# Kernel tuning notes

Measured on AMD Instinct MI355X. Metric: run time of the kernel, lower is better.

## Reference

```python
import jax, jax.numpy as jnp
import numpy as np

STATE_DIM = 16
MEAS_DIM = 8
T = 500_000


def setup_inputs() -> dict:
    key = jax.random.key(0)
    k1, k2 = jax.random.split(key)
    measurements = jax.random.normal(k1, (T, MEAS_DIM, 1), dtype=jnp.float32)
    # F contracted slightly below identity so the 500k-step recursion stays stable
    F = 0.95 * jnp.eye(STATE_DIM, dtype=jnp.float32) \
        + 0.01 * jax.random.normal(k2, (STATE_DIM, STATE_DIM), dtype=jnp.float32)
    H = jnp.eye(MEAS_DIM, STATE_DIM, dtype=jnp.float32)  # matches nn.Parameter(torch.eye(m, n))
    Q = jnp.eye(STATE_DIM, dtype=jnp.float32)
    R = jnp.eye(MEAS_DIM, dtype=jnp.float32)
    return {"measurements": measurements, "F": F, "H": H, "Q": Q, "R": R}


def reference(measurements, F, H, Q, R):
    n = F.shape[0]
    I = jnp.eye(n, dtype=F.dtype)
    x0 = jnp.zeros((n, 1), dtype=F.dtype)   # self.x init
    P0 = jnp.eye(n, dtype=F.dtype)          # self.P init

    def step(carry, z):
        x, P = carry
        # predict
        x = F @ x
        P = F @ P @ F.T + Q
        # update
        y = z - H @ x                         # (m,1) innovation
        S = H @ P @ H.T + R                   # (m,m) innovation covariance
        K = P @ H.T @ jnp.linalg.inv(S)       # (n,m) Kalman gain (faithful to torch.linalg.inv)
        x = x + K @ y
        P = (I - K @ H) @ P
        return (x, P), x

    _, states = jax.lax.scan(step, (x0, P0), measurements)
    return states  # (T, n, 1)
```

## Files before the change

### kernel.cpp

```cpp
#include <hip/hip_runtime.h>


#define TT 500000
#define T0 40
#define L1 32
#define NCHUNK 15624
#define GH 16
#define OWN 32
#define NBLK2 489

#define OFF_A    0
#define OFF_KR   256
#define OFF_AL   512
#define OFF_KH   784

#define FENCE_LDS() do { \
  asm volatile("s_waitcnt lgkmcnt(0)" ::: "memory"); \
  __builtin_amdgcn_sched_barrier(0); \
} while (0)

#define FMACDPP(d, x, a, S) \
  asm("v_fmac_f32_dpp %0, %1, %2 row_ror:" #S " row_mask:0xf bank_mask:0xf" \
      : "+v"(d) : "v"(x), "v"(a))
#define MULDPPD(d, x, a, dep, S) \
  asm("v_mul_f32_dpp %0, %1, %2 row_ror:" #S " row_mask:0xf bank_mask:0xf" \
      : "=v"(d) : "v"(x), "v"(a), "v"(dep))

__device__ __forceinline__ float rlf(float v, int lane) {
  return __int_as_float(__builtin_amdgcn_readlane(__float_as_int(v), lane));
}
__device__ __forceinline__ float bpermf(int byteaddr, float v) {
  return __int_as_float(__builtin_amdgcn_ds_bpermute(byteaddr, __float_as_int(v)));
}
template<int CTL> __device__ __forceinline__ float dppf(float x) {
  return __int_as_float(__builtin_amdgcn_update_dpp(
      0, __float_as_int(x), CTL, 0xF, 0xF, false));
}
#define QP1 0x39
#define QP2 0x4E
#define QP3 0x93

__device__ __forceinline__ int rot_dir() {
  int r = threadIdx.x & 15;
  int m = __builtin_amdgcn_update_dpp(0, r, 0x121, 0xF, 0xF, false);
  return (m - r) & 15;
}
__device__ __forceinline__ float mv16(const float a[16], float x) {
  float s0 = a[0] * x;
  float s1, s2, s3;
  MULDPPD(s1, x, a[1], s0, 1);
  MULDPPD(s2, x, a[2], s0, 2);
  MULDPPD(s3, x, a[3], s0, 3);
  FMACDPP(s0, x, a[4], 4);   FMACDPP(s1, x, a[5], 5);
  FMACDPP(s2, x, a[6], 6);   FMACDPP(s3, x, a[7], 7);
  FMACDPP(s0, x, a[8], 8);   FMACDPP(s1, x, a[9], 9);
  FMACDPP(s2, x, a[10], 10); FMACDPP(s3, x, a[11], 11);
  FMACDPP(s0, x, a[12], 12); FMACDPP(s1, x, a[13], 13);
  FMACDPP(s2, x, a[14], 14); FMACDPP(s3, x, a[15], 15);
  return (s0 + s1) + (s2 + s3);
}
__device__ __forceinline__ float stepAK(const float a[16], const float k8[8],
                                        float u, float zv) {
  float s0 = __builtin_fmaf(k8[0], zv, a[0] * u);
  float s1, s2, s3;
  MULDPPD(s1, u, a[1], s0, 1);
  MULDPPD(s2, u, a[2], s0, 2);
  MULDPPD(s3, u, a[3], s0, 3);
  FMACDPP(s0, u, a[4], 4);   FMACDPP(s1, u, a[5], 5);
  FMACDPP(s2, u, a[6], 6);   FMACDPP(s3, u, a[7], 7);
  FMACDPP(s0, u, a[8], 8);   FMACDPP(s1, u, a[9], 9);
  FMACDPP(s2, u, a[10], 10); FMACDPP(s3, u, a[11], 11);
  FMACDPP(s0, u, a[12], 12); FMACDPP(s1, u, a[13], 13);
  FMACDPP(s2, u, a[14], 14); FMACDPP(s3, u, a[15], 15);
  FMACDPP(s1, zv, k8[1], 1); FMACDPP(s2, zv, k8[2], 2);
  FMACDPP(s3, zv, k8[3], 3); FMACDPP(s0, zv, k8[4], 4);
  FMACDPP(s1, zv, k8[5], 5); FMACDPP(s2, zv, k8[6], 6);
  FMACDPP(s3, zv, k8[7], 7);
  return (s0 + s1) + (s2 + s3);
}
__device__ __forceinline__ void load16(const float* p, int r, float d[16]) {
  #pragma unroll
  for (int j = 0; j < 4; ++j) {
    float4 t = ((const float4*)p)[r*4 + j];
    d[4*j] = t.x; d[4*j+1] = t.y; d[4*j+2] = t.z; d[4*j+3] = t.w;
  }
}
__device__ __forceinline__ void loadkrf(const float* p, int r, float k8[8]) {
  float kr[16];
  load16(p, r, kr);
  #pragma unroll
  for (int i = 0; i < 8; ++i) k8[i] = kr[i] + kr[i + 8];
}
__device__ __forceinline__ void loadz(const float* __restrict__ z, int s0_,
                                      int rr, float zr[L1]) {
  const float* zp = z + (size_t)s0_ * 8 + (rr & 7);
  if (s0_ + L1 <= TT) {
    #pragma unroll
    for (int t = 0; t < L1; ++t) zr[t] = zp[t * 8];
  } else {
    #pragma unroll
    for (int t = 0; t < L1; ++t) {
      const float* q = (s0_ + t < TT) ? (zp + t * 8) : z;
      zr[t] = *q;
    }
  }
}

__global__ __launch_bounds__(64) void kf_ricc(
    const float* __restrict__ Fg, const float* __restrict__ Qg,
    const float* __restrict__ Rg, float* __restrict__ ws)
{
  const int l  = threadIdx.x;
  const int r4 = l >> 2;
  const int q  = l & 3;
  const int c4 = q * 4;
  const int dir = rot_dir();

  __shared__ float Ps[16][20], Pbs[16][20], Ms[16][20];
  __shared__ float KsL[16][8];

  float frow[16];
  #pragma unroll
  for (int k = 0; k < 16; ++k) frow[k] = Fg[r4*16 + k];
  float4 ftr[16];
  #pragma unroll
  for (int d = 0; d < 4; ++d) {
    #pragma unroll
    for (int jp = 0; jp < 4; ++jp) {
      int col = 4*((q + d) & 3) + jp;
      ftr[d*4+jp] = make_float4(Fg[(c4+0)*16 + col], Fg[(c4+1)*16 + col],
                                Fg[(c4+2)*16 + col], Fg[(c4+3)*16 + col]);
    }
  }
  float4 qreg = *(const float4*)&Qg[r4*16 + c4];
  float rcol[8];
  {
    int cc = l & 7;
    #pragma unroll
    for (int i = 0; i < 8; ++i) rcol[i] = Rg[i*8 + cc];
  }
  *(float4*)&Ps[r4][c4] = make_float4(r4==c4 ?1.f:0.f, r4==c4+1?1.f:0.f,
                                      r4==c4+2?1.f:0.f, r4==c4+3?1.f:0.f);
  const int  cidx = (l < 8) ? l : ((l < 24) ? (l - 8) : (l & 7));
  const bool isS  = (l < 8);
  const bool isB  = (l >= 8 && l < 24);
  const int  bj   = l - 8;
  const int  ba   = (8 + r4) << 2;
  float v[8];
  FENCE_LDS();

  for (int t = 0; t < T0; ++t) {
    float m0=0.f,m1=0.f,m2=0.f,m3=0.f;
    #pragma unroll
    for (int k = 0; k < 16; ++k) {
      float4 pk = *(const float4*)&Ps[k][c4];
      float f = frow[k];
      m0 += f*pk.x; m1 += f*pk.y; m2 += f*pk.z; m3 += f*pk.w;
    }
    float g1x=dppf<QP1>(m0), g1y=dppf<QP1>(m1), g1z=dppf<QP1>(m2), g1w=dppf<QP1>(m3);
    float g2x=dppf<QP2>(m0), g2y=dppf<QP2>(m1), g2z=dppf<QP2>(m2), g2w=dppf<QP2>(m3);
    float g3x=dppf<QP3>(m0), g3y=dppf<QP3>(m1), g3z=dppf<QP3>(m2), g3w=dppf<QP3>(m3);
    const float mq[4][4] = {{m0,m1,m2,m3},{g1x,g1y,g1z,g1w},
                            {g2x,g2y,g2z,g2w},{g3x,g3y,g3z,g3w}};
    float b0=qreg.x, b1=qreg.y, b2=qreg.z, b3=qreg.w;
    #pragma unroll
    for (int d = 0; d < 4; ++d) {
      #pragma unroll
      for (int jp = 0; jp < 4; ++jp) {
        float mm = mq[d][jp];
        float4 ft = ftr[d*4+jp];
        b0 += mm*ft.x; b1 += mm*ft.y; b2 += mm*ft.z; b3 += mm*ft.w;
      }
    }
    float4 pb = make_float4(b0,b1,b2,b3);
    *(float4*)&Pbs[r4][c4] = pb;
    FENCE_LDS();
    #pragma unroll
    for (int i = 0; i < 8; ++i)
      v[i] = Pbs[i][cidx] + (isS ? rcol[i] : 0.f);
    #pragma unroll
    for (int p = 0; p < 8; ++p) {
      float piv = rlf(v[p], p);
      float rc  = __builtin_amdgcn_rcpf(piv);
      float fi[8];
      #pragma unroll
      for (int i = 0; i < 8; ++i) fi[i] = rlf(v[i], p) * rc;
      #pragma unroll
      for (int i = 0; i < 8; ++i) if (i != p) v[i] -= fi[i] * v[p];
    }
    {
      float dv[8];
      #pragma unroll
      for (int i = 0; i < 8; ++i) dv[i] = __builtin_amdgcn_rcpf(rlf(v[i], i));
      #pragma unroll
      for (int i = 0; i < 8; ++i) v[i] *= dv[i];
    }
    if (isB) {
      #pragma unroll
      for (int i = 0; i < 8; ++i) ws[OFF_KH + t*128 + bj*8 + i] = v[i];
    }
    float kk[8];
    #pragma unroll
    for (int i = 0; i < 8; ++i) kk[i] = bpermf(ba, v[i]);
    float4 pn = pb;
    #pragma unroll
    for (int k = 0; k < 8; ++k) {
      float4 pr = *(const float4*)&Pbs[k][c4];
      float kv = kk[k];
      pn.x -= kv*pr.x; pn.y -= kv*pr.y; pn.z -= kv*pr.z; pn.w -= kv*pr.w;
    }
    *(float4*)&Ps[r4][c4] = pn;
    FENCE_LDS();
  }

  if (isB) {
    #pragma unroll
    for (int i = 0; i < 8; ++i) KsL[bj][i] = v[i];
  }
  float kk[8];
  #pragma unroll
  for (int i = 0; i < 8; ++i) kk[i] = bpermf(ba, v[i]);
  float a[4];
  #pragma unroll
  for (int j = 0; j < 4; ++j) {
    float s = Fg[r4*16 + c4 + j];
    #pragma unroll
    for (int k = 0; k < 8; ++k) s -= kk[k] * Fg[k*16 + c4 + j];
    a[j] = s;
  }
  *(float4*)&Ms[r4][c4] = make_float4(a[0],a[1],a[2],a[3]);
  #pragma unroll
  for (int j = 0; j < 4; ++j) {
    int c = c4 + j;
    int s = ((c - r4) * dir) & 15;
    ws[OFF_A + r4*16 + s] = a[j];
  }
  FENCE_LDS();
  if (l < 16) {
    #pragma unroll
    for (int s = 0; s < 16; ++s) {
      int c = (l + s*dir) & 15;
      ws[OFF_KR + l*16 + s] = (c < 8) ? KsL[l][c] : 0.f;
    }
  }
  FENCE_LDS();
  for (int n = 0; n < 5; ++n) {
    float (*src)[20] = (n & 1) ? Pbs : Ms;
    float (*dst)[20] = (n & 1) ? Ms : Pbs;
    float b[4] = {0.f, 0.f, 0.f, 0.f};
    #pragma unroll
    for (int k = 0; k < 16; ++k) {
      float m = src[r4][k];
      const float* p = &src[k][c4];
      b[0] += m*p[0]; b[1] += m*p[1]; b[2] += m*p[2]; b[3] += m*p[3];
    }
    FENCE_LDS();
    dst[r4][c4]=b[0]; dst[r4][c4+1]=b[1]; dst[r4][c4+2]=b[2]; dst[r4][c4+3]=b[3];
    FENCE_LDS();
    if (n == 4) {
      #pragma unroll
      for (int j = 0; j < 4; ++j) {
        int c = c4 + j;
        int s = ((c - r4) * dir) & 15;
        ws[OFF_AL + r4*16 + s] = b[j];
      }
    }
  }
}

__global__ __launch_bounds__(768) void kf_scan(
    const float* __restrict__ z, const float* __restrict__ Fg,
    float* __restrict__ ws, float* __restrict__ out)
{
  const int tid = threadIdx.x;
  const int bid = blockIdx.x;
  const int r = tid & 15;
  const int g = tid >> 4;

  __shared__ float ueL[48 * 16];
  __shared__ float X0s[16];

  float a[16], krf[8];
  load16(&ws[OFF_A], r, a);
  loadkrf(&ws[OFF_KR], r, krf);

  float zr[L1];
  int myc = -1, mylen = 0, mys0 = 0;

  if (g < GH) {
    if (bid == 0) {
      if (g == 0) {
        float f[16];
        #pragma unroll
        for (int i = 0; i < 16; ++i) f[i] = Fg[r*16 + i];
        const float4* zb = (const float4*)z + r;
        const float4* kh = (const float4*)&ws[OFF_KH] + r*2;
        float x = 0.f;
        float4 d0 = zb[0], d1 = zb[16];
        float4 ka0 = kh[0],  kb0 = kh[1];
        float4 ka1 = kh[32], kb1 = kh[33];
        for (int b = 0; b < T0/8; ++b) {
          float4 nx = (b + 2 < T0/8) ? zb[(b+2)*16] : make_float4(0.f,0.f,0.f,0.f);
          #pragma unroll
          for (int j = 0; j < 8; ++j) {
            const int t = b*8 + j;
            float p0=0.f,p1=0.f,p2=0.f,p3=0.f;
            #pragma unroll
            for (int k = 0; k < 16; k += 4) {
              p0 += f[k]   * __shfl(x, k, 16);
              p1 += f[k+1] * __shfl(x, k+1, 16);
              p2 += f[k+2] * __shfl(x, k+2, 16);
              p3 += f[k+3] * __shfl(x, k+3, 16);
            }
            float xp = (p0+p1)+(p2+p3);
            float z0=__shfl(d0.x,2*j,16),   z1=__shfl(d0.y,2*j,16);
            float z2=__shfl(d0.z,2*j,16),   z3=__shfl(d0.w,2*j,16);
            float z4=__shfl(d0.x,2*j+1,16), z5=__shfl(d0.y,2*j+1,16);
            float z6=__shfl(d0.z,2*j+1,16), z7=__shfl(d0.w,2*j+1,16);
            float acc = xp;
            acc += ka0.x * (z0 - __shfl(xp,0,16));
            acc += ka0.y * (z1 - __shfl(xp,1,16));
            acc += ka0.z * (z2 - __shfl(xp,2,16));
            acc += ka0.w * (z3 - __shfl(xp,3,16));
            acc += kb0.x * (z4 - __shfl(xp,4,16));
            acc += kb0.y * (z5 - __shfl(xp,5,16));
            acc += kb0.z * (z6 - __shfl(xp,6,16));
            acc += kb0.w * (z7 - __shfl(xp,7,16));
            x = acc;
            out[t*16 + r] = x;
            ka0 = ka1; kb0 = kb1;
            if (t + 2 < T0) { ka1 = kh[(t+2)*32]; kb1 = kh[(t+2)*32 + 1]; }
          }
          d0 = d1; d1 = nx;
        }
        X0s[r] = x;
      }
    } else {
      int cg = bid*OWN - GH + g;
      int s0_ = T0 + cg*L1;
      loadz(z, s0_, r, zr);
      float u = 0.f;
      #pragma unroll
      for (int t = 0; t < L1; ++t) u = stepAK(a, krf, u, zr[t]);
      ueL[g*16 + r] = u;
    }
  } else {
    int k = g - GH;
    int c = bid*OWN + k;
    if (c < NCHUNK) {
      myc = c;
      mys0 = T0 + c*L1;
      mylen = min(mys0 + L1, TT) - mys0;
      loadz(z, mys0, r, zr);
      float u = 0.f;
      #pragma unroll
      for (int t = 0; t < L1; ++t) {
        if (t >= mylen) break;
        u = stepAK(a, krf, u, zr[t]);
        zr[t] = u;
      }
      ueL[g*16 + r] = u;
    }
  }
  float al[16];
  load16(&ws[OFF_AL], r, al);
  __syncthreads();

  if (myc >= 0) {
    const int k = myc - bid*OWN;
    float v = 0.f;
    if (myc >= GH) {
      float w[GH];
      #pragma unroll
      for (int m = 0; m < GH; ++m) w[m] = ueL[(k + m)*16 + r];
      #pragma unroll
      for (int m = 0; m < GH; ++m) v = mv16(al, v) + w[m];
    } else {
      for (int j = -1; j < myc; ++j) {
        float val = (j < 0) ? X0s[r] : ueL[(GH + j)*16 + r];
        v = mv16(al, v) + val;
      }
    }
    float w = v;
    #pragma unroll
    for (int t = 0; t < L1; ++t) {
      if (t >= mylen) break;
      w = mv16(a, w);
      out[(size_t)(mys0 + t)*16 + r] = zr[t] + w;
    }
  }
}

extern "C" void kernel_launch(void* const* d_in, const int* in_sizes, int n_in,
                              void* d_out, int out_size, void* d_ws, size_t ws_size,
                              hipStream_t stream) {
  const float* z  = (const float*)d_in[0];
  const float* Fg = (const float*)d_in[1];
  const float* Qg = (const float*)d_in[3];
  const float* Rg = (const float*)d_in[4];
  float* out = (float*)d_out;
  float* ws  = (float*)d_ws;

  kf_ricc<<<1, 64, 0, stream>>>(Fg, Qg, Rg, ws);
  kf_scan<<<NBLK2, 768, 0, stream>>>(z, Fg, ws, out);
}
```

Before: 84.75 us.

## Process two consecutive chunks per thread group to halve block count and halo work

```diff
diff --git a/kernel.cpp b/kernel.cpp
--- a/kernel.cpp
+++ b/kernel.cpp
@@ -6,8 +6,8 @@
 #define L1 32
 #define NCHUNK 15624
 #define GH 16
-#define OWN 32
-#define NBLK2 489
+#define OWN 64
+#define NBLK2 245
 
 #define OFF_A    0
 #define OFF_KR   256
@@ -277,15 +277,15 @@
   const int r = tid & 15;
   const int g = tid >> 4;
 
-  __shared__ float ueL[48 * 16];
+  __shared__ float ueL[(GH + OWN) * 16];
   __shared__ float X0s[16];
 
   float a[16], krf[8];
   load16(&ws[OFF_A], r, a);
   loadkrf(&ws[OFF_KR], r, krf);
 
-  float zr[L1];
-  int myc = -1, mylen = 0, mys0 = 0;
+  float zrA[L1], zrB[L1];
+  int cA = -1, cB = -1, lenB = 0, s0A = 0, s0B = 0;
 
   if (g < GH) {
     if (bid == 0) {
@@ -338,55 +338,75 @@
     } else {
       int cg = bid*OWN - GH + g;
       int s0_ = T0 + cg*L1;
-      loadz(z, s0_, r, zr);
+      loadz(z, s0_, r, zrA);
       float u = 0.f;
       #pragma unroll
-      for (int t = 0; t < L1; ++t) u = stepAK(a, krf, u, zr[t]);
+      for (int t = 0; t < L1; ++t) u = stepAK(a, krf, u, zrA[t]);
       ueL[g*16 + r] = u;
     }
   } else {
     int k = g - GH;
-    int c = bid*OWN + k;
-    if (c < NCHUNK) {
-      myc = c;
-      mys0 = T0 + c*L1;
-      mylen = min(mys0 + L1, TT) - mys0;
-      loadz(z, mys0, r, zr);
+    cA = bid*OWN + 2*k;
+    if (cA < NCHUNK) {
+      s0A = T0 + cA*L1;
+      loadz(z, s0A, r, zrA);
       float u = 0.f;
       #pragma unroll
       for (int t = 0; t < L1; ++t) {
-        if (t >= mylen) break;
-        u = stepAK(a, krf, u, zr[t]);
-        zr[t] = u;
-      }
-      ueL[g*16 + r] = u;
+        u = stepAK(a, krf, u, zrA[t]);
+        zrA[t] = u;
+      }
+      ueL[(GH + 2*k)*16 + r] = u;
+      cB = cA + 1;
+      if (cB < NCHUNK) {
+        s0B = s0A + L1;
+        lenB = min(s0B + L1, TT) - s0B;
+        loadz(z, s0B, r, zrB);
+        u = 0.f;
+        #pragma unroll
+        for (int t = 0; t < L1; ++t) {
+          if (t >= lenB) break;
+          u = stepAK(a, krf, u, zrB[t]);
+          zrB[t] = u;
+        }
+        ueL[(GH + 2*k + 1)*16 + r] = u;
+      }
+    } else {
+      cA = -1;
     }
   }
   float al[16];
   load16(&ws[OFF_AL], r, al);
   __syncthreads();
 
-  if (myc >= 0) {
-    const int k = myc - bid*OWN;
+  if (cA >= 0) {
+    const int k2 = 2*(g - GH);
     float v = 0.f;
-    if (myc >= GH) {
-      float w[GH];
-      #pragma unroll
-      for (int m = 0; m < GH; ++m) w[m] = ueL[(k + m)*16 + r];
-      #pragma unroll
-      for (int m = 0; m < GH; ++m) v = mv16(al, v) + w[m];
+    if (cA >= GH) {
+      float w16[GH];
+      #pragma unroll
+      for (int m = 0; m < GH; ++m) w16[m] = ueL[(k2 + m)*16 + r];
+      #pragma unroll
+      for (int m = 0; m < GH; ++m) v = mv16(al, v) + w16[m];
     } else {
-      for (int j = -1; j < myc; ++j) {
-        float val = (j < 0) ? X0s[r] : ueL[(GH + j)*16 + r];
-        v = mv16(al, v) + val;
-      }
+      v = X0s[r];
+      for (int j = 0; j < cA; ++j)
+        v = mv16(al, v) + ueL[(GH + j)*16 + r];
     }
     float w = v;
     #pragma unroll
     for (int t = 0; t < L1; ++t) {
-      if (t >= mylen) break;
       w = mv16(a, w);
-      out[(size_t)(mys0 + t)*16 + r] = zr[t] + w;
+      out[(size_t)(s0A + t)*16 + r] = zrA[t] + w;
+    }
+    if (cB < NCHUNK && cB >= 0) {
+      w = zrA[L1-1] + w;
+      #pragma unroll
+      for (int t = 0; t < L1; ++t) {
+        if (t >= lenB) break;
+        w = mv16(a, w);
+        out[(size_t)(s0B + t)*16 + r] = zrB[t] + w;
+      }
     }
   }
 }
```

Measured after the change: 76.67 us. 9.5% less time.
